# Performance work log

Hardware: AMD Instinct MI355X
Metric: run time of the kernel (lower is better)

Reference implementation:

```python
import jax, jax.numpy as jnp
import numpy as np

N_NODES = 100000
N_EDGES = 6400000
HID = 32


def setup_inputs() -> dict:
    key = jax.random.key(0)
    ks = jax.random.split(key, 24)
    inp = {
        "x_G": jax.random.normal(ks[0], (N_NODES, 1), dtype=jnp.float32),
        "edge_index_G": jax.random.randint(ks[1], (2, N_EDGES), 0, N_NODES, dtype=jnp.int32),
        "x_H": jax.random.normal(ks[2], (N_NODES, 1), dtype=jnp.float32),
        "edge_index_H": jax.random.randint(ks[3], (2, N_EDGES), 0, N_NODES, dtype=jnp.int32),
    }
    ki = 4
    for i in range(3):
        d_in = 1 if i == 0 else HID
        inp[f"W1_{i}"] = jax.random.normal(ks[ki], (d_in, HID), dtype=jnp.float32) / np.sqrt(d_in); ki += 1
        inp[f"b1_{i}"] = jnp.zeros((HID,), dtype=jnp.float32)
        inp[f"W2_{i}"] = jax.random.normal(ks[ki], (HID, HID), dtype=jnp.float32) / np.sqrt(HID); ki += 1
        inp[f"b2_{i}"] = jnp.zeros((HID,), dtype=jnp.float32)
    inp["Wc1"] = jax.random.normal(ks[ki], (2 * HID, HID), dtype=jnp.float32) / np.sqrt(2 * HID); ki += 1
    inp["bc1"] = jnp.zeros((HID,), dtype=jnp.float32)
    inp["Wc2"] = jax.random.normal(ks[ki], (HID, 1), dtype=jnp.float32) / np.sqrt(HID); ki += 1
    inp["bc2"] = jnp.zeros((1,), dtype=jnp.float32)
    return inp


def _encode(x, edge_index, layers):
    n = x.shape[0]
    src, dst = edge_index[0], edge_index[1]
    for (W1, b1, W2, b2) in layers:
        # GIN aggregation: sum of neighbor messages scattered to targets; eps = 0
        agg = jax.ops.segment_sum(x[src], dst, num_segments=n)  # [N, d]
        h = x + agg  # (1 + eps) * x + agg with eps = 0
        h = jax.nn.relu(h @ W1 + b1) @ W2 + b2  # GIN MLP
        x = jax.nn.relu(h)  # outer F.relu in encode loop
    return jnp.sum(x, axis=0, keepdims=True)  # global_add_pool, single graph -> [1, HID]


def reference(x_G, edge_index_G, x_H, edge_index_H,
              W1_0, b1_0, W2_0, b2_0,
              W1_1, b1_1, W2_1, b2_1,
              W1_2, b1_2, W2_2, b2_2,
              Wc1, bc1, Wc2, bc2):
    layers = [(W1_0, b1_0, W2_0, b2_0),
              (W1_1, b1_1, W2_1, b2_1),
              (W1_2, b1_2, W2_2, b2_2)]
    h_G = _encode(x_G, edge_index_G, layers)
    h_H = _encode(x_H, edge_index_H, layers)
    combined = jnp.concatenate([h_G, h_H], axis=1)  # [1, 2*HID]
    out = jax.nn.relu(combined @ Wc1 + bc1) @ Wc2 + bc2
    return jax.nn.sigmoid(out)
```

## Files before the change

### kernel.cpp

```cpp
#include <hip/hip_runtime.h>
#include <hip/hip_bf16.h>
#include <math.h>
#include <string.h>

#define HID 32
#define PSHIFT 8
#define NPB (1 << PSHIFT)
#define MAXP 512
#define SLOTS 17408
#define SBITS 3
#define SBINS (1 << SBITS)
#define NBINS (NPB * SBINS)
#define COLBUF 6144
#define GS 32
#define HS_ROWS 32
typedef unsigned short u16;

__device__ inline float bf2f(u16 u) {
    unsigned v = ((unsigned)u) << 16;
    float f; memcpy(&f, &v, 4); return f;
}
__device__ inline u16 f2bf(float f) {
    unsigned x; memcpy(&x, &f, 4);
    unsigned r = x + 0x7fffu + ((x >> 16) & 1u);
    return (u16)(r >> 16);
}
__device__ inline void acc_bf8(float* a, uint4 w) {
    a[0] += bf2f((u16)(w.x & 0xffff)); a[1] += bf2f((u16)(w.x >> 16));
    a[2] += bf2f((u16)(w.y & 0xffff)); a[3] += bf2f((u16)(w.y >> 16));
    a[4] += bf2f((u16)(w.z & 0xffff)); a[5] += bf2f((u16)(w.z >> 16));
    a[6] += bf2f((u16)(w.w & 0xffff)); a[7] += bf2f((u16)(w.w >> 16));
}

__global__ void zero_kernel(float* __restrict__ p, int n) {
    int i = blockIdx.x * blockDim.x + threadIdx.x;
    if (i < n) p[i] = 0.f;
}
__global__ void init_gcur(int* __restrict__ gcur, int P) {
    int b = blockIdx.x * blockDim.x + threadIdx.x;
    if (b < P) gcur[b * GS] = b * SLOTS;
}

__global__ void partition_edges(const int* __restrict__ src, const int* __restrict__ dst,
                                int* __restrict__ gcur, unsigned* __restrict__ staged,
                                int E, int P) {
    __shared__ int h[4][MAXP];
    __shared__ int hbase[MAXP];
    __shared__ int cur[MAXP];
    __shared__ int gbase[MAXP];
    __shared__ unsigned sortedv[4096];
    __shared__ u16 bktid[4096];
    __shared__ int wsums[4];
    __shared__ int sTotal;
    int t = threadIdx.x, wid = t >> 6, lane = t & 63;
    for (int i = t; i < 4 * MAXP; i += 256) (&h[0][0])[i] = 0;
    __syncthreads();

    int base = blockIdx.x * 4096;
    int4 S[4], D[4];
#pragma unroll
    for (int r = 0; r < 4; r++) {
        int e = base + r * 1024 + t * 4;
        if (e + 3 < E) {
            S[r] = *(const int4*)(src + e);
            D[r] = *(const int4*)(dst + e);
        } else {
            int s0[4], d0[4];
            for (int j = 0; j < 4; j++) {
                int ee = e + j;
                s0[j] = (ee < E) ? src[ee] : -1;
                d0[j] = (ee < E) ? dst[ee] : -1;
            }
            S[r] = make_int4(s0[0], s0[1], s0[2], s0[3]);
            D[r] = make_int4(d0[0], d0[1], d0[2], d0[3]);
        }
        if (D[r].x >= 0) atomicAdd(&h[wid][D[r].x >> PSHIFT], 1);
        if (D[r].y >= 0) atomicAdd(&h[wid][D[r].y >> PSHIFT], 1);
        if (D[r].z >= 0) atomicAdd(&h[wid][D[r].z >> PSHIFT], 1);
        if (D[r].w >= 0) atomicAdd(&h[wid][D[r].w >> PSHIFT], 1);
    }
    __syncthreads();

    int b0 = 2 * t, b1 = 2 * t + 1;
    int t0 = (b0 < P) ? (h[0][b0] + h[1][b0] + h[2][b0] + h[3][b0]) : 0;
    int t1 = (b1 < P) ? (h[0][b1] + h[1][b1] + h[2][b1] + h[3][b1]) : 0;
    int s = t0 + t1;
    int incl = s;
#pragma unroll
    for (int off = 1; off < 64; off <<= 1) {
        int u = __shfl_up(incl, off, 64);
        if (lane >= off) incl += u;
    }
    if (lane == 63) wsums[wid] = incl;
    __syncthreads();
    int woff = 0;
#pragma unroll
    for (int w = 0; w < 4; w++) if (w < wid) woff += wsums[w];
    int excl = woff + incl - s;
    if (b0 < P) { hbase[b0] = excl;      cur[b0] = excl; }
    if (b1 < P) { hbase[b1] = excl + t0; cur[b1] = excl + t0; }
    if (b0 < P && t0) gbase[b0] = atomicAdd(&gcur[b0 * GS], t0);
    if (b1 < P && t1) gbase[b1] = atomicAdd(&gcur[b1 * GS], t1);
    if (t == 255) sTotal = excl + s;
    __syncthreads();

#pragma unroll
    for (int r = 0; r < 4; r++) {
        int ss[4] = { S[r].x, S[r].y, S[r].z, S[r].w };
        int dd[4] = { D[r].x, D[r].y, D[r].z, D[r].w };
#pragma unroll
        for (int j = 0; j < 4; j++) {
            int d = dd[j];
            if (d >= 0) {
                int bk = d >> PSHIFT;
                int pos = atomicAdd(&cur[bk], 1);
                sortedv[pos] = ((unsigned)(d & (NPB - 1)) << 17) | (unsigned)ss[j];
                bktid[pos]   = (u16)bk;
            }
        }
    }
    __syncthreads();

    int total = sTotal;
    for (int i = t; i < total; i += 256) {
        int bk = bktid[i];
        int addr = gbase[bk] + (i - hbase[bk]);
        if (addr < (bk + 1) * SLOTS)
            staged[addr] = sortedv[i];
    }
}

__global__ void scan_buckets(const int* __restrict__ gcur, int* __restrict__ colbase,
                             int* __restrict__ rowptr, int P, int N) {
    __shared__ int wsums[4];
    int t = threadIdx.x, wid = t >> 6, lane = t & 63;
    int b0 = 2 * t, b1 = 2 * t + 1;
    int c0 = 0, c1 = 0;
    if (b0 < P) { c0 = gcur[b0 * GS] - b0 * SLOTS; if (c0 > SLOTS) c0 = SLOTS; }
    if (b1 < P) { c1 = gcur[b1 * GS] - b1 * SLOTS; if (c1 > SLOTS) c1 = SLOTS; }
    int s = c0 + c1;
    int incl = s;
#pragma unroll
    for (int off = 1; off < 64; off <<= 1) {
        int u = __shfl_up(incl, off, 64);
        if (lane >= off) incl += u;
    }
    if (lane == 63) wsums[wid] = incl;
    __syncthreads();
    int woff = 0;
#pragma unroll
    for (int w = 0; w < 4; w++) if (w < wid) woff += wsums[w];
    int excl = woff + incl - s;
    if (b0 < P) colbase[b0] = excl;
    if (b1 < P) colbase[b1] = excl + c0;
    if (t == 255) {
        colbase[P] = excl + s;
        rowptr[N]  = excl + s;
    }
}

__global__ void sort_bucket(const unsigned* __restrict__ staged, const int* __restrict__ gcur,
                            const int* __restrict__ colbase,
                            int* __restrict__ rowptr, int* __restrict__ col, int N) {
    __shared__ int cnt[NBINS];
    __shared__ int wsum[4];
    __shared__ int sorted[SLOTS];
    int b = blockIdx.x;
    int t = threadIdx.x;
    int lane = t & 63, wid = t >> 6;
    int sBeg = b * SLOTS;
    int sEnd = gcur[b * GS]; if (sEnd > sBeg + SLOTS) sEnd = sBeg + SLOTS;
    int total = sEnd - sBeg;
    int colStart = colbase[b];
    int nodeBase = b << PSHIFT;

    for (int i = t; i < NBINS; i += 256) cnt[i] = 0;
    __syncthreads();
    for (int i = sBeg + t; i < sEnd; i += 256) {
        unsigned w = staged[i];
        int key = (int)((w >> 17) << SBITS) | (int)((w & 0x1FFFFu) >> 14);
        atomicAdd(&cnt[key], 1);
    }
    __syncthreads();

    int loc[SBINS]; int tot = 0;
#pragma unroll
    for (int k = 0; k < SBINS; k++) { loc[k] = tot; tot += cnt[(t << SBITS) + k]; }
    int incl = tot;
#pragma unroll
    for (int off = 1; off < 64; off <<= 1) {
        int u = __shfl_up(incl, off, 64);
        if (lane >= off) incl += u;
    }
    if (lane == 63) wsum[wid] = incl;
    __syncthreads();
    int woff = 0;
#pragma unroll
    for (int w = 0; w < 4; w++) if (w < wid) woff += wsum[w];
    int excl = woff + incl - tot;
    int node = nodeBase + t;
    if (node < N) rowptr[node] = colStart + excl;
#pragma unroll
    for (int k = 0; k < SBINS; k++) cnt[(t << SBITS) + k] = excl + loc[k];
    __syncthreads();

    for (int i = sBeg + t; i < sEnd; i += 256) {
        unsigned w = staged[i];
        int key = (int)((w >> 17) << SBITS) | (int)((w & 0x1FFFFu) >> 14);
        int pos = atomicAdd(&cnt[key], 1);
        sorted[pos] = (int)(w & 0x1FFFFu);
    }
    __syncthreads();
    for (int i = t; i < total; i += 256)
        col[colStart + i] = sorted[i];
}

__global__ void mlp0_fused(const int* __restrict__ rowptr, const int* __restrict__ col,
                           const float* __restrict__ x0,
                           const float* __restrict__ W1, const float* __restrict__ b1,
                           const float* __restrict__ W2, const float* __restrict__ b2,
                           u16* __restrict__ out, int n) {
    __shared__ float sW1[HID], sb1[HID], sW2[HID * HID], sb2[HID];
    int t = threadIdx.x;
    if (t < HID) { sW1[t] = W1[t]; sb1[t] = b1[t]; sb2[t] = b2[t]; }
    for (int i = t; i < HID * HID; i += blockDim.x) sW2[i] = W2[i];
    __syncthreads();
    int node = blockIdx.x * blockDim.x + t;
    if (node >= n) return;
    int beg = rowptr[node], end = rowptr[node + 1];
    float s0 = 0.f, s1 = 0.f, s2 = 0.f, s3 = 0.f;
    int j = beg;
    for (; j + 8 <= end; j += 8) {
        int c0 = col[j+0], c1 = col[j+1], c2 = col[j+2], c3 = col[j+3];
        int c4 = col[j+4], c5 = col[j+5], c6 = col[j+6], c7 = col[j+7];
        float v0 = x0[c0], v1 = x0[c1], v2 = x0[c2], v3 = x0[c3];
        float v4 = x0[c4], v5 = x0[c5], v6 = x0[c6], v7 = x0[c7];
        s0 += v0; s1 += v1; s2 += v2; s3 += v3;
        s0 += v4; s1 += v5; s2 += v6; s3 += v7;
    }
    for (; j < end; j++) s0 += x0[col[j]];
    float v = x0[node] + ((s0 + s1) + (s2 + s3));
    float h[HID];
#pragma unroll
    for (int k = 0; k < HID; k++) h[k] = fmaxf(fmaf(v, sW1[k], sb1[k]), 0.f);
    float o[HID];
#pragma unroll
    for (int k = 0; k < HID; k++) o[k] = sb2[k];
#pragma unroll
    for (int k = 0; k < HID; k++) {
        float hj = h[k];
#pragma unroll
        for (int m = 0; m < HID; m++) o[m] = fmaf(hj, sW2[k * HID + m], o[m]);
    }
    u16* op = out + (size_t)node * HID;
#pragma unroll
    for (int c = 0; c < 4; c++) {
        union { u16 u[8]; uint4 v; } pk;
#pragma unroll
        for (int i = 0; i < 8; i++) pk.u[i] = f2bf(fmaxf(o[c * 8 + i], 0.f));
        *(uint4*)(op + c * 8) = pk.v;
    }
}

template <bool REDUCE>
__global__ void mlp_fused(const int* __restrict__ rowptr, const int* __restrict__ col,
                          const u16* __restrict__ xin,
                          const float* __restrict__ W1, const float* __restrict__ b1,
                          const float* __restrict__ W2, const float* __restrict__ b2,
                          u16* __restrict__ xout, float* __restrict__ hsum, int n) {
    __shared__ float sW1[HID * HID], sb1[HID], sW2[HID * HID], sb2[HID];
    __shared__ int colbuf[COLBUF];
    __shared__ float red[4][HID];
    int t = threadIdx.x;
    for (int i = t; i < HID * HID; i += blockDim.x) { sW1[i] = W1[i]; sW2[i] = W2[i]; }
    if (t < HID) { sb1[t] = b1[t]; sb2[t] = b2[t]; }

    int firstNode = blockIdx.x * 64;
    int lastNode  = firstNode + 64; if (lastNode > n) lastNode = n;
    int blockStart = (firstNode < n) ? rowptr[firstNode] : 0;
    int blockEnd   = (firstNode < n) ? rowptr[lastNode] : 0;
    int stagedCnt = blockEnd - blockStart; if (stagedCnt > COLBUF) stagedCnt = COLBUF;
    for (int i = t; i < stagedCnt; i += 256) colbuf[i] = col[blockStart + i];
    __syncthreads();

    int node = firstNode + (t >> 2);
    int q    = t & 3;
    int lane = t & 63;
    int base = lane & ~3;
    bool active = node < n;

    float va[8];
#pragma unroll
    for (int i = 0; i < 8; i++) va[i] = 0.f;
    if (active) {
        int beg = rowptr[node], end = rowptr[node + 1];
        const u16* xq = xin + (q << 3);
        float a0[8], a1[8], a2[8], a3[8];
        {
            uint4 w = *(const uint4*)(xq + ((size_t)node << 5));
#pragma unroll
            for (int i = 0; i < 8; i++) a0[i] = a1[i] = a2[i] = a3[i] = 0.f;
            acc_bf8(a0, w);
        }
        int jSplit = blockStart + stagedCnt; if (jSplit > end) jSplit = end;
        int j = beg;
        for (; j + 8 <= jSplit; j += 8) {
            int lj = j - blockStart;
            int c0 = colbuf[lj+0], c1 = colbuf[lj+1], c2 = colbuf[lj+2], c3 = colbuf[lj+3];
            int c4 = colbuf[lj+4], c5 = colbuf[lj+5], c6 = colbuf[lj+6], c7 = colbuf[lj+7];
            uint4 w0 = *(const uint4*)(xq + ((size_t)c0 << 5));
            uint4 w1 = *(const uint4*)(xq + ((size_t)c1 << 5));
            uint4 w2 = *(const uint4*)(xq + ((size_t)c2 << 5));
            uint4 w3 = *(const uint4*)(xq + ((size_t)c3 << 5));
            uint4 w4 = *(const uint4*)(xq + ((size_t)c4 << 5));
            uint4 w5 = *(const uint4*)(xq + ((size_t)c5 << 5));
            uint4 w6 = *(const uint4*)(xq + ((size_t)c6 << 5));
            uint4 w7 = *(const uint4*)(xq + ((size_t)c7 << 5));
            acc_bf8(a0, w0); acc_bf8(a1, w1); acc_bf8(a2, w2); acc_bf8(a3, w3);
            acc_bf8(a0, w4); acc_bf8(a1, w5); acc_bf8(a2, w6); acc_bf8(a3, w7);
        }
        for (; j < jSplit; j++) {
            uint4 w = *(const uint4*)(xq + ((size_t)colbuf[j - blockStart] << 5));
            acc_bf8(a0, w);
        }
        for (; j < end; j++) {
            uint4 w = *(const uint4*)(xq + ((size_t)col[j] << 5));
            acc_bf8(a0, w);
        }
#pragma unroll
        for (int i = 0; i < 8; i++) va[i] = (a0[i] + a1[i]) + (a2[i] + a3[i]);
    }

    float h[8];
#pragma unroll
    for (int i = 0; i < 8; i++) h[i] = sb1[q * 8 + i];
#pragma unroll
    for (int k = 0; k < HID; k++) {
        float vk = __shfl(va[k & 7], base | (k >> 3), 64);
#pragma unroll
        for (int i = 0; i < 8; i++) h[i] = fmaf(vk, sW1[k * HID + q * 8 + i], h[i]);
    }
#pragma unroll
    for (int i = 0; i < 8; i++) h[i] = fmaxf(h[i], 0.f);

    float o[8];
#pragma unroll
    for (int i = 0; i < 8; i++) o[i] = sb2[q * 8 + i];
#pragma unroll
    for (int k = 0; k < HID; k++) {
        float hk = __shfl(h[k & 7], base | (k >> 3), 64);
#pragma unroll
        for (int i = 0; i < 8; i++) o[i] = fmaf(hk, sW2[k * HID + q * 8 + i], o[i]);
    }
#pragma unroll
    for (int i = 0; i < 8; i++) o[i] = fmaxf(o[i], 0.f);

    if (REDUCE) {
        if (!active) {
#pragma unroll
            for (int i = 0; i < 8; i++) o[i] = 0.f;
        }
#pragma unroll
        for (int i = 0; i < 8; i++) {
            float v = o[i];
            v += __shfl_xor(v, 4, 64);
            v += __shfl_xor(v, 8, 64);
            v += __shfl_xor(v, 16, 64);
            v += __shfl_xor(v, 32, 64);
            o[i] = v;
        }
        int wid = t >> 6;
        if (lane < 4) {
#pragma unroll
            for (int i = 0; i < 8; i++) red[wid][q * 8 + i] = o[i];
        }
        __syncthreads();
        if (t < HID) {
            float s = red[0][t] + red[1][t] + red[2][t] + red[3][t];
            atomicAdd(&hsum[(blockIdx.x & (HS_ROWS - 1)) * (2 * HID) + t], s);
        }
    } else if (active) {
        union { u16 u[8]; uint4 v; } pk;
#pragma unroll
        for (int i = 0; i < 8; i++) pk.u[i] = f2bf(o[i]);
        *(uint4*)(xout + ((size_t)node << 5) + (q << 3)) = pk.v;
    }
}

__global__ void head_kernel(const float* __restrict__ hsumP,
                            const float* __restrict__ Wc1, const float* __restrict__ bc1,
                            const float* __restrict__ Wc2, const float* __restrict__ bc2,
                            float* __restrict__ out) {
    __shared__ float hs[2 * HID];
    int t = threadIdx.x;
    if (t < 2 * HID) {
        float s = 0.f;
        for (int r = 0; r < HS_ROWS; r++) s += hsumP[r * (2 * HID) + t];
        hs[t] = s;
    }
    __syncthreads();
    float val = 0.f;
    if (t < HID) {
        float acc = bc1[t];
        for (int i = 0; i < 2 * HID; i++) acc = fmaf(hs[i], Wc1[i * HID + t], acc);
        val = fmaxf(acc, 0.f) * Wc2[t];
    }
    for (int off = 32; off >= 1; off >>= 1) val += __shfl_xor(val, off, 64);
    if (t == 0) out[0] = 1.f / (1.f + expf(-(val + bc2[0])));
}

extern "C" void kernel_launch(void* const* d_in, const int* in_sizes, int n_in,
                              void* d_out, int out_size, void* d_ws, size_t ws_size,
                              hipStream_t stream) {
    const float* xg[2] = { (const float*)d_in[0], (const float*)d_in[2] };
    const int*   eg[2] = { (const int*)d_in[1],   (const int*)d_in[3] };
    const float* W1[3] = { (const float*)d_in[4], (const float*)d_in[8],  (const float*)d_in[12] };
    const float* b1[3] = { (const float*)d_in[5], (const float*)d_in[9],  (const float*)d_in[13] };
    const float* W2[3] = { (const float*)d_in[6], (const float*)d_in[10], (const float*)d_in[14] };
    const float* b2[3] = { (const float*)d_in[7], (const float*)d_in[11], (const float*)d_in[15] };
    const float* Wc1 = (const float*)d_in[16];
    const float* bc1 = (const float*)d_in[17];
    const float* Wc2 = (const float*)d_in[18];
    const float* bc2 = (const float*)d_in[19];

    const int N = in_sizes[0];
    const int E = in_sizes[1] / 2;
    const int P = (N + NPB - 1) >> PSHIFT;

    u16*      B0      = (u16*)d_ws;
    u16*      B1      = B0 + (size_t)N * HID;
    float*    hsumP   = (float*)(B1 + (size_t)N * HID);
    int*      rowptr  = (int*)(hsumP + HS_ROWS * 2 * HID);
    int*      col     = rowptr + (N + 1);
    int*      colbase = col + (size_t)E;
    int*      gcur    = colbase + (P + 1);
    unsigned* staged  = (unsigned*)(gcur + (size_t)P * GS);

    const int TB = 256;
    dim3 blk(TB);
    int gN   = (N + TB - 1) / TB;
    int gE4k = (E + 4095) / 4096;
    int gN4  = ((size_t)N * 4 + TB - 1) / TB;
    int gP   = (P + TB - 1) / TB;

    zero_kernel<<<(HS_ROWS * 2 * HID + 255) / 256, 256, 0, stream>>>(hsumP, HS_ROWS * 2 * HID);

    for (int g = 0; g < 2; g++) {
        const float* x0  = xg[g];
        const int*   src = eg[g];
        const int*   dst = src + E;

        init_gcur<<<gP, blk, 0, stream>>>(gcur, P);
        partition_edges<<<gE4k, blk, 0, stream>>>(src, dst, gcur, staged, E, P);
        scan_buckets<<<1, blk, 0, stream>>>(gcur, colbase, rowptr, P, N);
        sort_bucket<<<P, blk, 0, stream>>>(staged, gcur, colbase, rowptr, col, N);

        mlp0_fused<<<gN, blk, 0, stream>>>(rowptr, col, x0, W1[0], b1[0], W2[0], b2[0], B0, N);

        mlp_fused<false><<<gN4, blk, 0, stream>>>(rowptr, col, B0, W1[1], b1[1], W2[1], b2[1],
                                                  B1, nullptr, N);

        mlp_fused<true><<<gN4, blk, 0, stream>>>(rowptr, col, B1, W1[2], b1[2], W2[2], b2[2],
                                                 nullptr, hsumP + g * HID, N);
    }

    head_kernel<<<1, 64, 0, stream>>>(hsumP, Wc1, bc1, Wc2, bc2, (float*)d_out);
}
```

Baseline: 640.8 us.

## Spread node gathers across more lanes in GIN layer kernels

```diff
diff --git a/kernel.cpp b/kernel.cpp
--- a/kernel.cpp
+++ b/kernel.cpp
@@ -11,9 +11,10 @@
 #define SBITS 3
 #define SBINS (1 << SBITS)
 #define NBINS (NPB * SBINS)
-#define COLBUF 6144
 #define GS 32
 #define HS_ROWS 32
+#define COLBUF 1536
+#define COLBUF0 6144
 typedef unsigned short u16;
 
 __device__ inline float bf2f(u16 u) {
@@ -25,11 +26,9 @@
     unsigned r = x + 0x7fffu + ((x >> 16) & 1u);
     return (u16)(r >> 16);
 }
-__device__ inline void acc_bf8(float* a, uint4 w) {
-    a[0] += bf2f((u16)(w.x & 0xffff)); a[1] += bf2f((u16)(w.x >> 16));
-    a[2] += bf2f((u16)(w.y & 0xffff)); a[3] += bf2f((u16)(w.y >> 16));
-    a[4] += bf2f((u16)(w.z & 0xffff)); a[5] += bf2f((u16)(w.z >> 16));
-    a[6] += bf2f((u16)(w.w & 0xffff)); a[7] += bf2f((u16)(w.w >> 16));
+__device__ inline void acc_bf2(float* a, unsigned w) {
+    a[0] += bf2f((u16)(w & 0xffff));
+    a[1] += bf2f((u16)(w >> 16));
 }
 
 __global__ void zero_kernel(float* __restrict__ p, int n) {
@@ -221,44 +220,61 @@
                            const float* __restrict__ W2, const float* __restrict__ b2,
                            u16* __restrict__ out, int n) {
     __shared__ float sW1[HID], sb1[HID], sW2[HID * HID], sb2[HID];
+    __shared__ int colbuf[COLBUF0];
     int t = threadIdx.x;
     if (t < HID) { sW1[t] = W1[t]; sb1[t] = b1[t]; sb2[t] = b2[t]; }
     for (int i = t; i < HID * HID; i += blockDim.x) sW2[i] = W2[i];
-    __syncthreads();
-    int node = blockIdx.x * blockDim.x + t;
-    if (node >= n) return;
-    int beg = rowptr[node], end = rowptr[node + 1];
-    float s0 = 0.f, s1 = 0.f, s2 = 0.f, s3 = 0.f;
-    int j = beg;
-    for (; j + 8 <= end; j += 8) {
-        int c0 = col[j+0], c1 = col[j+1], c2 = col[j+2], c3 = col[j+3];
-        int c4 = col[j+4], c5 = col[j+5], c6 = col[j+6], c7 = col[j+7];
-        float v0 = x0[c0], v1 = x0[c1], v2 = x0[c2], v3 = x0[c3];
-        float v4 = x0[c4], v5 = x0[c5], v6 = x0[c6], v7 = x0[c7];
-        s0 += v0; s1 += v1; s2 += v2; s3 += v3;
-        s0 += v4; s1 += v5; s2 += v6; s3 += v7;
-    }
-    for (; j < end; j++) s0 += x0[col[j]];
-    float v = x0[node] + ((s0 + s1) + (s2 + s3));
-    float h[HID];
-#pragma unroll
-    for (int k = 0; k < HID; k++) h[k] = fmaxf(fmaf(v, sW1[k], sb1[k]), 0.f);
-    float o[HID];
-#pragma unroll
-    for (int k = 0; k < HID; k++) o[k] = sb2[k];
+
+    int firstNode = blockIdx.x * 64;
+    int lastNode  = firstNode + 64; if (lastNode > n) lastNode = n;
+    int blockStart = (firstNode < n) ? rowptr[firstNode] : 0;
+    int blockEnd   = (firstNode < n) ? rowptr[lastNode] : 0;
+    int stagedCnt = blockEnd - blockStart; if (stagedCnt > COLBUF0) stagedCnt = COLBUF0;
+    for (int i = t; i < stagedCnt; i += 256) colbuf[i] = col[blockStart + i];
+    __syncthreads();
+
+    int node = firstNode + (t >> 2);
+    int q    = t & 3;
+    int lane = t & 63;
+    int base = lane & ~3;
+    bool active = node < n;
+
+    float s = 0.f;
+    if (active) {
+        int beg = rowptr[node], end = rowptr[node + 1];
+        int jSplit = blockStart + stagedCnt; if (jSplit > end) jSplit = end;
+        int j = beg + q;
+        for (; j + 12 < jSplit; j += 16) {
+            int c0 = colbuf[j - blockStart];
+            int c1 = colbuf[j + 4 - blockStart];
+            int c2 = colbuf[j + 8 - blockStart];
+            int c3 = colbuf[j + 12 - blockStart];
+            s += x0[c0]; s += x0[c1]; s += x0[c2]; s += x0[c3];
+        }
+        for (; j < jSplit; j += 4) s += x0[colbuf[j - blockStart]];
+        for (; j < end; j += 4) s += x0[col[j]];
+    }
+    s += __shfl_xor(s, 1, 64);
+    s += __shfl_xor(s, 2, 64);
+    float v = active ? (x0[node] + s) : 0.f;
+
+    float h[8];
+#pragma unroll
+    for (int i = 0; i < 8; i++) h[i] = fmaxf(fmaf(v, sW1[q * 8 + i], sb1[q * 8 + i]), 0.f);
+    float o[8];
+#pragma unroll
+    for (int i = 0; i < 8; i++) o[i] = sb2[q * 8 + i];
 #pragma unroll
     for (int k = 0; k < HID; k++) {
-        float hj = h[k];
-#pragma unroll
-        for (int m = 0; m < HID; m++) o[m] = fmaf(hj, sW2[k * HID + m], o[m]);
-    }
-    u16* op = out + (size_t)node * HID;
-#pragma unroll
-    for (int c = 0; c < 4; c++) {
-        union { u16 u[8]; uint4 v; } pk;
-#pragma unroll
-        for (int i = 0; i < 8; i++) pk.u[i] = f2bf(fmaxf(o[c * 8 + i], 0.f));
-        *(uint4*)(op + c * 8) = pk.v;
+        float hk = __shfl(h[k & 7], base | (k >> 3), 64);
+#pragma unroll
+        for (int i = 0; i < 8; i++) o[i] = fmaf(hk, sW2[k * HID + q * 8 + i], o[i]);
+    }
+    if (active) {
+        union { u16 u[8]; uint4 v4; } pk;
+#pragma unroll
+        for (int i = 0; i < 8; i++) pk.u[i] = f2bf(fmaxf(o[i], 0.f));
+        *(uint4*)(out + ((size_t)node << 5) + (q << 3)) = pk.v4;
     }
 }
 
@@ -275,32 +291,31 @@
     for (int i = t; i < HID * HID; i += blockDim.x) { sW1[i] = W1[i]; sW2[i] = W2[i]; }
     if (t < HID) { sb1[t] = b1[t]; sb2[t] = b2[t]; }
 
-    int firstNode = blockIdx.x * 64;
-    int lastNode  = firstNode + 64; if (lastNode > n) lastNode = n;
+    int firstNode = blockIdx.x * 16;
+    int lastNode  = firstNode + 16; if (lastNode > n) lastNode = n;
     int blockStart = (firstNode < n) ? rowptr[firstNode] : 0;
     int blockEnd   = (firstNode < n) ? rowptr[lastNode] : 0;
     int stagedCnt = blockEnd - blockStart; if (stagedCnt > COLBUF) stagedCnt = COLBUF;
     for (int i = t; i < stagedCnt; i += 256) colbuf[i] = col[blockStart + i];
     __syncthreads();
 
-    int node = firstNode + (t >> 2);
-    int q    = t & 3;
+    int node = firstNode + (t >> 4);
+    int q    = t & 15;
     int lane = t & 63;
-    int base = lane & ~3;
+    int base = lane & ~15;
     bool active = node < n;
 
-    float va[8];
-#pragma unroll
-    for (int i = 0; i < 8; i++) va[i] = 0.f;
+    float va[2];
+    va[0] = 0.f; va[1] = 0.f;
     if (active) {
         int beg = rowptr[node], end = rowptr[node + 1];
-        const u16* xq = xin + (q << 3);
-        float a0[8], a1[8], a2[8], a3[8];
+        const u16* xq = xin + (q << 1);
+        float a0[2], a1[2], a2[2], a3[2];
+#pragma unroll
+        for (int i = 0; i < 2; i++) a0[i] = a1[i] = a2[i] = a3[i] = 0.f;
         {
-            uint4 w = *(const uint4*)(xq + ((size_t)node << 5));
-#pragma unroll
-            for (int i = 0; i < 8; i++) a0[i] = a1[i] = a2[i] = a3[i] = 0.f;
-            acc_bf8(a0, w);
+            unsigned w = *(const unsigned*)(xq + ((size_t)node << 5));
+            acc_bf2(a0, w);
         }
         int jSplit = blockStart + stagedCnt; if (jSplit > end) jSplit = end;
         int j = beg;
@@ -308,71 +323,69 @@
             int lj = j - blockStart;
             int c0 = colbuf[lj+0], c1 = colbuf[lj+1], c2 = colbuf[lj+2], c3 = colbuf[lj+3];
             int c4 = colbuf[lj+4], c5 = colbuf[lj+5], c6 = colbuf[lj+6], c7 = colbuf[lj+7];
-            uint4 w0 = *(const uint4*)(xq + ((size_t)c0 << 5));
-            uint4 w1 = *(const uint4*)(xq + ((size_t)c1 << 5));
-            uint4 w2 = *(const uint4*)(xq + ((size_t)c2 << 5));
-            uint4 w3 = *(const uint4*)(xq + ((size_t)c3 << 5));
-            uint4 w4 = *(const uint4*)(xq + ((size_t)c4 << 5));
-            uint4 w5 = *(const uint4*)(xq + ((size_t)c5 << 5));
-            uint4 w6 = *(const uint4*)(xq + ((size_t)c6 << 5));
-            uint4 w7 = *(const uint4*)(xq + ((size_t)c7 << 5));
-            acc_bf8(a0, w0); acc_bf8(a1, w1); acc_bf8(a2, w2); acc_bf8(a3, w3);
-            acc_bf8(a0, w4); acc_bf8(a1, w5); acc_bf8(a2, w6); acc_bf8(a3, w7);
+            unsigned w0 = *(const unsigned*)(xq + ((size_t)c0 << 5));
+            unsigned w1 = *(const unsigned*)(xq + ((size_t)c1 << 5));
+            unsigned w2 = *(const unsigned*)(xq + ((size_t)c2 << 5));
+            unsigned w3 = *(const unsigned*)(xq + ((size_t)c3 << 5));
+            unsigned w4 = *(const unsigned*)(xq + ((size_t)c4 << 5));
+            unsigned w5 = *(const unsigned*)(xq + ((size_t)c5 << 5));
+            unsigned w6 = *(const unsigned*)(xq + ((size_t)c6 << 5));
+            unsigned w7 = *(const unsigned*)(xq + ((size_t)c7 << 5));
+            acc_bf2(a0, w0); acc_bf2(a1, w1); acc_bf2(a2, w2); acc_bf2(a3, w3);
+            acc_bf2(a0, w4); acc_bf2(a1, w5); acc_bf2(a2, w6); acc_bf2(a3, w7);
         }
         for (; j < jSplit; j++) {
-            uint4 w = *(const uint4*)(xq + ((size_t)colbuf[j - blockStart] << 5));
-            acc_bf8(a0, w);
+            unsigned w = *(const unsigned*)(xq + ((size_t)colbuf[j - blockStart] << 5));
+            acc_bf2(a0, w);
         }
         for (; j < end; j++) {
-            uint4 w = *(const uint4*)(xq + ((size_t)col[j] << 5));
-            acc_bf8(a0, w);
-        }
-#pragma unroll
-        for (int i = 0; i < 8; i++) va[i] = (a0[i] + a1[i]) + (a2[i] + a3[i]);
-    }
-
-    float h[8];
-#pragma unroll
-    for (int i = 0; i < 8; i++) h[i] = sb1[q * 8 + i];
+            unsigned w = *(const unsigned*)(xq + ((size_t)col[j] << 5));
+            acc_bf2(a0, w);
+        }
+#pragma unroll
+        for (int i = 0; i < 2; i++) va[i] = (a0[i] + a1[i]) + (a2[i] + a3[i]);
+    }
+
+    float h[2];
+#pragma unroll
+    for (int i = 0; i < 2; i++) h[i] = sb1[q * 2 + i];
 #pragma unroll
     for (int k = 0; k < HID; k++) {
-        float vk = __shfl(va[k & 7], base | (k >> 3), 64);
-#pragma unroll
-        for (int i = 0; i < 8; i++) h[i] = fmaf(vk, sW1[k * HID + q * 8 + i], h[i]);
-    }
-#pragma unroll
-    for (int i = 0; i < 8; i++) h[i] = fmaxf(h[i], 0.f);
-
-    float o[8];
-#pragma unroll
-    for (int i = 0; i < 8; i++) o[i] = sb2[q * 8 + i];
+        float vk = __shfl(va[k & 1], base | (k >> 1), 64);
+#pragma unroll
+        for (int i = 0; i < 2; i++) h[i] = fmaf(vk, sW1[k * HID + q * 2 + i], h[i]);
+    }
+#pragma unroll
+    for (int i = 0; i < 2; i++) h[i] = fmaxf(h[i], 0.f);
+
+    float o[2];
+#pragma unroll
+    for (int i = 0; i < 2; i++) o[i] = sb2[q * 2 + i];
 #pragma unroll
     for (int k = 0; k < HID; k++) {
-        float hk = __shfl(h[k & 7], base | (k >> 3), 64);
-#pragma unroll
-        for (int i = 0; i < 8; i++) o[i] = fmaf(hk, sW2[k * HID + q * 8 + i], o[i]);
-    }
-#pragma unroll
-    for (int i = 0; i < 8; i++) o[i] = fmaxf(o[i], 0.f);
+        float hk = __shfl(h[k & 1], base | (k >> 1), 64);
+#pragma unroll
+        for (int i = 0; i < 2; i++) o[i] = fmaf(hk, sW2[k * HID + q * 2 + i], o[i]);
+    }
+#pragma unroll
+    for (int i = 0; i < 2; i++) o[i] = fmaxf(o[i], 0.f);
 
     if (REDUCE) {
         if (!active) {
 #pragma unroll
-            for (int i = 0; i < 8; i++) o[i] = 0.f;
-        }
-#pragma unroll
-        for (int i = 0; i < 8; i++) {
+            for (int i = 0; i < 2; i++) o[i] = 0.f;
+        }
+#pragma unroll
+        for (int i = 0; i < 2; i++) {
             float v = o[i];
-            v += __shfl_xor(v, 4, 64);
-            v += __shfl_xor(v, 8, 64);
             v += __shfl_xor(v, 16, 64);
             v += __shfl_xor(v, 32, 64);
             o[i] = v;
         }
         int wid = t >> 6;
-        if (lane < 4) {
-#pragma unroll
-            for (int i = 0; i < 8; i++) red[wid][q * 8 + i] = o[i];
+        if (lane < 16) {
+#pragma unroll
+            for (int i = 0; i < 2; i++) red[wid][lane * 2 + i] = o[i];
         }
         __syncthreads();
         if (t < HID) {
@@ -380,10 +393,9 @@
             atomicAdd(&hsum[(blockIdx.x & (HS_ROWS - 1)) * (2 * HID) + t], s);
         }
     } else if (active) {
-        union { u16 u[8]; uint4 v; } pk;
-#pragma unroll
-        for (int i = 0; i < 8; i++) pk.u[i] = f2bf(o[i]);
-        *(uint4*)(xout + ((size_t)node << 5) + (q << 3)) = pk.v;
+        union { u16 u[2]; unsigned w; } pk;
+        pk.u[0] = f2bf(o[0]); pk.u[1] = f2bf(o[1]);
+        *(unsigned*)(xout + ((size_t)node << 5) + (q << 1)) = pk.w;
     }
 }
 
@@ -438,9 +450,9 @@
 
     const int TB = 256;
     dim3 blk(TB);
-    int gN   = (N + TB - 1) / TB;
     int gE4k = (E + 4095) / 4096;
-    int gN4  = ((size_t)N * 4 + TB - 1) / TB;
+    int gN64 = (N + 63) / 64;
+    int gN16 = (N + 15) / 16;
     int gP   = (P + TB - 1) / TB;
 
     zero_kernel<<<(HS_ROWS * 2 * HID + 255) / 256, 256, 0, stream>>>(hsumP, HS_ROWS * 2 * HID);
@@ -455,13 +467,13 @@
         scan_buckets<<<1, blk, 0, stream>>>(gcur, colbase, rowptr, P, N);
         sort_bucket<<<P, blk, 0, stream>>>(staged, gcur, colbase, rowptr, col, N);
 
-        mlp0_fused<<<gN, blk, 0, stream>>>(rowptr, col, x0, W1[0], b1[0], W2[0], b2[0], B0, N);
-
-        mlp_fused<false><<<gN4, blk, 0, stream>>>(rowptr, col, B0, W1[1], b1[1], W2[1], b2[1],
-                                                  B1, nullptr, N);
-
-        mlp_fused<true><<<gN4, blk, 0, stream>>>(rowptr, col, B1, W1[2], b1[2], W2[2], b2[2],
-                                                 nullptr, hsumP + g * HID, N);
+        mlp0_fused<<<gN64, blk, 0, stream>>>(rowptr, col, x0, W1[0], b1[0], W2[0], b2[0], B0, N);
+
+        mlp_fused<false><<<gN16, blk, 0, stream>>>(rowptr, col, B0, W1[1], b1[1], W2[1], b2[1],
+                                                   B1, nullptr, N);
+
+        mlp_fused<true><<<gN16, blk, 0, stream>>>(rowptr, col, B1, W1[2], b1[2], W2[2], b2[2],
+                                                  nullptr, hsumP + g * HID, N);
     }
 
     head_kernel<<<1, 64, 0, stream>>>(hsumP, Wc1, bc1, Wc2, bc2, (float*)d_out);
```

New measurement: 654.6 us. 2.2% more time.
